# Kernel optimization log

Measured on AMD Instinct MI355X. Metric: run time of the kernel, lower is better.

Reference implementation:

```python
import jax, jax.numpy as jnp
import numpy as np
import math

B, H, M, L, D = 4, 8, 512, 2048, 64   # batch, heads, block len, span, head dim
RAMP = 64                              # adapt_span_len (soft-mask ramp size)


def setup_inputs() -> dict:
    key = jax.random.key(0)
    ks = jax.random.split(key, 5)
    BH = B * H
    KL = M + L
    return {
        "query": jax.random.normal(ks[0], (BH, M, D), jnp.float32),
        "key_": jax.random.normal(ks[1], (BH, KL, D), jnp.float32),
        "value": jax.random.normal(ks[2], (BH, KL, D), jnp.float32),
        "key_pe": jax.random.normal(ks[3], (1, D, L), jnp.float32) * 0.02,
        "current_val": jax.random.uniform(ks[4], (H, 1, 1), jnp.float32, minval=0.3, maxval=0.9),
    }


def reference(query, key_, value, key_pe, current_val):
    BH, Mq, Dh = query.shape
    KL = key_.shape[1]
    Lw = KL - Mq  # attention span
    nb = BH // current_val.shape[0]  # batch size (heads folded into leading dim)

    # full scores then unskew: band[b, i, j] = scores[b, i, i + j]
    scores = jnp.einsum('bmd,bnd->bmn', query, key_)              # (BH, M, M+L)
    rows = jnp.arange(Mq)[:, None]                                # (M, 1)
    band_idx = rows + jnp.arange(Lw)[None, :]                     # (M, L)
    attn = scores[:, rows, band_idx]                              # (BH, M, L)

    # relative position bias, scale, softmax
    attn = attn + jnp.einsum('bmd,dl->bml', query, key_pe[0])
    attn = attn / math.sqrt(Dh)
    attn = jax.nn.softmax(attn, axis=-1)

    # adaptive span soft mask (per head) + renormalization
    template = jnp.arange(1 - Lw, 1, dtype=attn.dtype)            # (L,) = linspace(1-L, 0, L)
    mask = jnp.clip((template + current_val * Lw) / RAMP + 1.0, 0.0, 1.0)  # (H, 1, L)
    attn4 = attn.reshape(nb, -1, Mq, Lw) * mask[None]             # (B, H, M, L)
    attn4 = attn4 / (attn4.sum(-1, keepdims=True) + 1e-8)
    attn = attn4.reshape(BH, Mq, Lw)

    # skew back to (BH, M, M+L) and contract with values
    skewed = jnp.zeros((BH, Mq, KL), attn.dtype).at[:, rows, band_idx].set(attn)
    out = jnp.einsum('bmn,bnd->bmd', skewed, value)               # (BH, M, D)
    return out
```

## Files before the change

### kernel.cpp

```cpp
#include <hip/hip_runtime.h>
#include <math.h>

typedef _Float16 half_t;
typedef _Float16 half8 __attribute__((ext_vector_type(8)));
typedef _Float16 half4 __attribute__((ext_vector_type(4)));
typedef _Float16 half2v __attribute__((ext_vector_type(2)));
typedef float f32x2 __attribute__((ext_vector_type(2)));
typedef float f32x4 __attribute__((ext_vector_type(4)));
typedef float f32x16 __attribute__((ext_vector_type(16)));
typedef unsigned int uint4v __attribute__((ext_vector_type(4)));

#define MFMA_S(a, b, c) __builtin_amdgcn_mfma_f32_32x32x16_f16((a), (b), (c), 0, 0, 0)

static constexpr int kM  = 512;
static constexpr int kD  = 64;
static constexpr int kKL = 2560;
static constexpr int kL  = 2048;
static constexpr int WS_VC  = 0;
static constexpr int WS_PET = WS_VC + 5242880;
static constexpr size_t WS_ZP_B = 10747904;
static constexpr size_t WS_PO_B = WS_ZP_B + 262144;

__global__ __launch_bounds__(256) void prep_tr(const float* __restrict__ v,
    const float* __restrict__ pe, half_t* __restrict__ ws) {
  __shared__ float ls[64 * 72];
  const int b = blockIdx.x, t = threadIdx.x;
  const bool isV = (b < 1280);
  int bh = 0, kt = 0, b3 = 0;
  const float* src; int sstride;
  if (isV) {
    bh = b / 40; kt = b % 40;
    src = v + (size_t)(bh * 2560 + kt * 64) * 64; sstride = 64;
  } else {
    b3 = b - 1280;
    src = pe + (size_t)b3 * 64; sstride = 2048;
  }
  const int rr = t >> 4, cq = (t & 15) * 4;
#pragma unroll
  for (int p = 0; p < 4; ++p) {
    const float4 x = *(const float4*)(src + (size_t)(p * 16 + rr) * sstride + cq);
    *(float4*)(ls + (p * 16 + rr) * 72 + cq) = x;
  }
  __syncthreads();
  const int oc = t >> 2, ch = t & 3;
  half_t tmp[16];
#pragma unroll
  for (int i2 = 0; i2 < 16; ++i2) tmp[i2] = (half_t)ls[(ch * 16 + i2) * 72 + oc];
  half_t* o;
  if (isV) {
    o = ws + WS_VC + (size_t)bh * 163840 + ((kt << 1) + (ch >> 1)) * 2048 + oc * 32 + ((ch & 1) << 4);
  } else {
    o = ws + WS_PET + ((size_t)b3 * 64 + oc) * 64 + ch * 16;
  }
  ((int4*)o)[0] = ((int4*)tmp)[0];
  ((int4*)o)[1] = ((int4*)tmp)[1];
}

__global__ __launch_bounds__(256, 2) void attn_kernel(
    const float* __restrict__ qg, const float* __restrict__ kg,
    const half_t* __restrict__ ws, const float* __restrict__ cvp,
    float* __restrict__ po, float* __restrict__ zp) {

  __shared__ __align__(16) char smem[43008];
  half_t* lsh = (half_t*)smem;

  const int tid  = threadIdx.x;
  const int lane = tid & 63;
  const int w    = tid >> 6;
  const int c32  = lane & 31;
  const int h    = lane >> 5;

  const int id = blockIdx.x;
  const int bh = ((id & 7) << 2) | (id >> 7);
  const int mid = (id >> 3) & 15;
  const int mb = mid & 3, sp = mid >> 2;
  const int m0 = mb << 7;
  const int g0 = sp * 17;

  const float cvl = cvp[bh & 7] * 2048.0f - 2047.0f;
  const float cvO = cvl * 0.015625f + 1.0f;

  const float*  kbF = kg + (size_t)bh * (kKL * kD);
  const half_t* vcb = ws + WS_VC + (size_t)bh * (kKL * kD);
  const half_t* pet = ws + WS_PET;

  const float QS = 0.125f * 1.4426950408889634f;
  const float* qrowF = qg + (size_t)(bh * kM + m0 + 32 * w + c32) * kD;
  half8 bq[4];
#pragma unroll
  for (int t = 0; t < 4; ++t) {
    const float4 qa = *(const float4*)(qrowF + t * 16 + h * 8);
    const float4 qb = *(const float4*)(qrowF + t * 16 + h * 8 + 4);
    bq[t] = half8{ (half_t)(qa.x * QS), (half_t)(qa.y * QS),
                   (half_t)(qa.z * QS), (half_t)(qa.w * QS),
                   (half_t)(qb.x * QS), (half_t)(qb.y * QS),
                   (half_t)(qb.z * QS), (half_t)(qb.w * QS) };
  }

  float* stfF = (float*)(smem + 9216) + w * 2112 + c32 * 66;

  float4 stgKa, stgKb;
  auto issueK = [&](int gg) {
    const int r = tid >> 3, seg = tid & 7;
    const int krow = m0 + (gg << 5) + r;
    const float* kp = kbF + (size_t)krow * kD + seg * 8;
    stgKa = *(const float4*)kp;
    stgKb = *(const float4*)(kp + 4);
  };
  auto commitK = [&](int gg) {
    const int sK = (gg & 1) * 2304;
    const int r = tid >> 3, seg = tid & 7;
    half_t tk[8];
    tk[0] = (half_t)stgKa.x; tk[1] = (half_t)stgKa.y;
    tk[2] = (half_t)stgKa.z; tk[3] = (half_t)stgKa.w;
    tk[4] = (half_t)stgKb.x; tk[5] = (half_t)stgKb.y;
    tk[6] = (half_t)stgKb.z; tk[7] = (half_t)stgKb.w;
    *(int4*)(lsh + sK + r * 72 + seg * 8) = *(int4*)tk;
  };

  auto loadV = [&](int gg, int4* vf) {
    const half_t* vp = vcb + (size_t)((m0 >> 5) + gg) * 2048;
#pragma unroll
    for (int dh = 0; dh < 2; ++dh)
#pragma unroll
      for (int kt = 0; kt < 2; ++kt)
        vf[dh * 2 + kt] = *(const int4*)(vp + (32 * dh + c32) * 32 + kt * 16 + h * 8);
  };

  auto petLoad = [&](int wb, half8* p) {
    int l = wb + c32; l = l < 0 ? 0 : (l > kL - 1 ? kL - 1 : l);
    const half_t* pp = pet + (size_t)l * kD;
#pragma unroll
    for (int t = 0; t < 4; ++t) p[t] = *(const half8*)(pp + t * 16 + h * 8);
  };
  auto peMFMA = [&](const half8* p) -> f32x16 {
    f32x16 a = {};
#pragma unroll
    for (int t = 0; t < 4; ++t) a = MFMA_S(p[t], bq[t], a);
    return a;
  };
  auto stripWrite = [&](int wb, const f32x16& a) {
    const int allone  = (wb >= 0) && (wb + 31 <= kL - 1) && (wb + cvl >= 0.0f);
    const int allzero = (wb > kL - 1) || (wb + 31 < 0) || ((float)(wb + 31) + cvl <= -64.0f);
#pragma unroll
    for (int reg = 0; reg < 16; ++reg) {
      const int lr = (reg & 3) + 8 * (reg >> 2) + 4 * h;
      const int l  = wb + lr;
      float bl;
      if (allzero) bl = -HUGE_VALF;
      else if (allone) bl = a[reg];
      else {
        const float mk = fminf(fmaxf((float)l * 0.015625f + cvO, 0.0f), 1.0f);
        const float lg = __builtin_amdgcn_logf(mk);
        bl = ((unsigned)l < (unsigned)kL) ? a[reg] + lg : -HUGE_VALF;
      }
      stfF[(l + c32) & 63] = bl;
    }
  };

  issueK(g0);
  const int B0 = (g0 << 5) - 32 * w;
  {
    half8 pq[4];
    petLoad(B0 - 32, pq); stripWrite(B0 - 32, peMFMA(pq));
    petLoad(B0,      pq); stripWrite(B0,      peMFMA(pq));
  }
  commitK(g0);
  __syncthreads();

  float zmc = 0.0f;
  f32x16 o0 = {}, o1 = {};

  half8 pp[4];
  int4 vf[4];
  for (int t = 0; t < 17; ++t) {
    const int g = g0 + t;
    const bool more = (t < 16);
    const int B = (g << 5) - 32 * w;
    if (more) {
      issueK(g + 1);
      petLoad(B + 32, pp);
    }
    loadV(g, vf);

    const int sK = (g & 1) * 2304;

    f32x16 s;
#pragma unroll
    for (int q = 0; q < 4; ++q) {
      const int base = (B + 8 * q + 4 * h) & 63;
      const f32x2 lo = *(const f32x2*)(stfF + base);
      const f32x2 hi = *(const f32x2*)(stfF + base + 2);
      s[4 * q + 0] = lo.x; s[4 * q + 1] = lo.y;
      s[4 * q + 2] = hi.x; s[4 * q + 3] = hi.y;
    }

    half8 ak[4];
#pragma unroll
    for (int kt = 0; kt < 4; ++kt)
      ak[kt] = *(const half8*)(lsh + sK + c32 * 72 + kt * 16 + h * 8);

#pragma unroll
    for (int kt = 0; kt < 4; ++kt) s = MFMA_S(ak[kt], bq[kt], s);

    float pm[16];
#pragma unroll
    for (int reg = 0; reg < 16; ++reg) pm[reg] = __builtin_amdgcn_exp2f(s[reg]);
    {
      const float t0 = (pm[0] + pm[1]) + (pm[2] + pm[3]);
      const float t1 = (pm[4] + pm[5]) + (pm[6] + pm[7]);
      const float t2 = (pm[8] + pm[9]) + (pm[10] + pm[11]);
      const float t3 = (pm[12] + pm[13]) + (pm[14] + pm[15]);
      zmc += (t0 + t1) + (t2 + t3);
    }
    unsigned Wp[8];
#pragma unroll
    for (int q = 0; q < 8; ++q)
      Wp[q] = __builtin_bit_cast(unsigned,
                __builtin_amdgcn_cvt_pkrtz(pm[2 * q], pm[2 * q + 1]));
    const auto r0 = __builtin_amdgcn_permlane32_swap(Wp[0], Wp[2], false, false);
    const auto r1 = __builtin_amdgcn_permlane32_swap(Wp[1], Wp[3], false, false);
    const auto r2 = __builtin_amdgcn_permlane32_swap(Wp[4], Wp[6], false, false);
    const auto r3 = __builtin_amdgcn_permlane32_swap(Wp[5], Wp[7], false, false);
    const uint4v u0 = { (unsigned)r0[0], (unsigned)r1[0], (unsigned)r0[1], (unsigned)r1[1] };
    const uint4v u1 = { (unsigned)r2[0], (unsigned)r3[0], (unsigned)r2[1], (unsigned)r3[1] };
    const half8 pb0 = __builtin_bit_cast(half8, u0);
    const half8 pb1 = __builtin_bit_cast(half8, u1);

    o0 = MFMA_S(__builtin_bit_cast(half8, vf[0]), pb0, o0);
    o0 = MFMA_S(__builtin_bit_cast(half8, vf[1]), pb1, o0);
    o1 = MFMA_S(__builtin_bit_cast(half8, vf[2]), pb0, o1);
    o1 = MFMA_S(__builtin_bit_cast(half8, vf[3]), pb1, o1);

    if (more) {
      stripWrite(B + 32, peMFMA(pp));
      commitK(g + 1);
    }
    __syncthreads();
  }

  float* Ow = (float*)smem + (size_t)w * 2176;
#pragma unroll
  for (int q = 0; q < 4; ++q) {
    *(f32x4*)(Ow + c32 * 68 + 0  + 8 * q + 4 * h) =
        f32x4{o0[q * 4], o0[q * 4 + 1], o0[q * 4 + 2], o0[q * 4 + 3]};
    *(f32x4*)(Ow + c32 * 68 + 32 + 8 * q + 4 * h) =
        f32x4{o1[q * 4], o1[q * 4 + 1], o1[q * 4 + 2], o1[q * 4 + 3]};
  }
  zmc += __shfl_xor(zmc, 32);
  const int rowbase = bh * kM + m0 + 32 * w;
  if (lane < 32) zp[(size_t)sp * 16384 + rowbase + c32] = zmc;
  __syncthreads();
  float* pob = po + ((size_t)sp * 16384 + rowbase) * 64;
#pragma unroll
  for (int u = 0; u < 8; ++u) {
    const int row = u * 4 + (lane >> 4);
    const int d4 = (lane & 15) << 2;
    *(f32x4*)(pob + (size_t)row * 64 + d4) = *(const f32x4*)(Ow + row * 68 + d4);
  }
}

__global__ __launch_bounds__(256) void norm_kernel(const float* __restrict__ zp,
    const float* __restrict__ po, float* __restrict__ out) {
  const int i = blockIdx.x * 256 + threadIdx.x;
  const int row = i >> 4, d4 = (i & 15) << 2;
  const float z = zp[row] + zp[16384 + row] + zp[32768 + row] + zp[49152 + row];
  const float inv = 1.0f / (z + 1e-20f);
  f32x4 a = *(const f32x4*)(po + (size_t)row * 64 + d4);
  const f32x4 b = *(const f32x4*)(po + 1048576u + (size_t)row * 64 + d4);
  const f32x4 c = *(const f32x4*)(po + 2097152u + (size_t)row * 64 + d4);
  const f32x4 d = *(const f32x4*)(po + 3145728u + (size_t)row * 64 + d4);
  a = a + b + c + d;
  *(f32x4*)(out + (size_t)row * 64 + d4) = a * inv;
}

extern "C" void kernel_launch(void* const* d_in, const int* in_sizes, int n_in,
                              void* d_out, int out_size, void* d_ws, size_t ws_size,
                              hipStream_t stream) {
  (void)in_sizes; (void)n_in; (void)out_size; (void)ws_size;
  const float* q  = (const float*)d_in[0];
  const float* k  = (const float*)d_in[1];
  const float* v  = (const float*)d_in[2];
  const float* pe = (const float*)d_in[3];
  const float* cv = (const float*)d_in[4];
  half_t* ws = (half_t*)d_ws;
  float* out = (float*)d_out;
  float* zp = (float*)((char*)d_ws + WS_ZP_B);
  float* po = (float*)((char*)d_ws + WS_PO_B);

  prep_tr<<<1312, 256, 0, stream>>>(v, pe, ws);
  attn_kernel<<<512, 256, 0, stream>>>(q, k, ws, cv, po, zp);
  norm_kernel<<<1024, 256, 0, stream>>>(zp, po, out);
}
```

Baseline: 133.6 us.

## Pre-convert K to fp16 and register-double-buffer K/V without per-step barriers

Adds a prep kernel that converts all of K to fp16 in the workspace. The attention kernel now loads K fragments straight from global into registers instead of staging them through shared memory. The main loop is unrolled by two with ping-pong register buffers for K, V and the position-embedding fragments, which removes the per-iteration __syncthreads. The cost is an extra kernel launch, a full extra read and write pass over K, and higher register pressure. K rows are also re-read from global/L2 by each wave instead of being shared through LDS.

```diff
diff --git a/kernel.cpp b/kernel.cpp
--- a/kernel.cpp
+++ b/kernel.cpp
@@ -16,10 +16,24 @@
 static constexpr int kD  = 64;
 static constexpr int kKL = 2560;
 static constexpr int kL  = 2048;
-static constexpr int WS_VC  = 0;
+static constexpr int WS_KH  = 0;
+static constexpr int WS_VC  = 5242880;
 static constexpr int WS_PET = WS_VC + 5242880;
-static constexpr size_t WS_ZP_B = 10747904;
+static constexpr size_t WS_ZP_B = 21233664;
 static constexpr size_t WS_PO_B = WS_ZP_B + 262144;
+
+__global__ __launch_bounds__(256) void prep_kc(const float* __restrict__ k,
+    half_t* __restrict__ ws) {
+  const int i = blockIdx.x * 256 + threadIdx.x;
+  const float* src = k + (size_t)i * 8;
+  half_t* dst = ws + WS_KH + (size_t)i * 8;
+  const float4 a = ((const float4*)src)[0];
+  const float4 b = ((const float4*)src)[1];
+  half_t tt[8];
+  tt[0] = (half_t)a.x; tt[1] = (half_t)a.y; tt[2] = (half_t)a.z; tt[3] = (half_t)a.w;
+  tt[4] = (half_t)b.x; tt[5] = (half_t)b.y; tt[6] = (half_t)b.z; tt[7] = (half_t)b.w;
+  *(int4*)dst = *(int4*)tt;
+}
 
 __global__ __launch_bounds__(256) void prep_tr(const float* __restrict__ v,
     const float* __restrict__ pe, half_t* __restrict__ ws) {
@@ -57,12 +71,11 @@
 }
 
 __global__ __launch_bounds__(256, 2) void attn_kernel(
-    const float* __restrict__ qg, const float* __restrict__ kg,
-    const half_t* __restrict__ ws, const float* __restrict__ cvp,
-    float* __restrict__ po, float* __restrict__ zp) {
-
-  __shared__ __align__(16) char smem[43008];
-  half_t* lsh = (half_t*)smem;
+    const float* __restrict__ qg, const half_t* __restrict__ ws,
+    const float* __restrict__ cvp, float* __restrict__ po,
+    float* __restrict__ zp) {
+
+  __shared__ __align__(16) char smem[34816];
 
   const int tid  = threadIdx.x;
   const int lane = tid & 63;
@@ -80,7 +93,7 @@
   const float cvl = cvp[bh & 7] * 2048.0f - 2047.0f;
   const float cvO = cvl * 0.015625f + 1.0f;
 
-  const float*  kbF = kg + (size_t)bh * (kKL * kD);
+  const half_t* khb = ws + WS_KH + (size_t)bh * (kKL * kD);
   const half_t* vcb = ws + WS_VC + (size_t)bh * (kKL * kD);
   const half_t* pet = ws + WS_PET;
 
@@ -97,37 +110,22 @@
                    (half_t)(qb.z * QS), (half_t)(qb.w * QS) };
   }
 
-  float* stfF = (float*)(smem + 9216) + w * 2112 + c32 * 66;
-
-  float4 stgKa, stgKb;
-  auto issueK = [&](int gg) {
-    const int r = tid >> 3, seg = tid & 7;
-    const int krow = m0 + (gg << 5) + r;
-    const float* kp = kbF + (size_t)krow * kD + seg * 8;
-    stgKa = *(const float4*)kp;
-    stgKb = *(const float4*)(kp + 4);
-  };
-  auto commitK = [&](int gg) {
-    const int sK = (gg & 1) * 2304;
-    const int r = tid >> 3, seg = tid & 7;
-    half_t tk[8];
-    tk[0] = (half_t)stgKa.x; tk[1] = (half_t)stgKa.y;
-    tk[2] = (half_t)stgKa.z; tk[3] = (half_t)stgKa.w;
-    tk[4] = (half_t)stgKb.x; tk[5] = (half_t)stgKb.y;
-    tk[6] = (half_t)stgKb.z; tk[7] = (half_t)stgKb.w;
-    *(int4*)(lsh + sK + r * 72 + seg * 8) = *(int4*)tk;
-  };
-
-  auto loadV = [&](int gg, int4* vf) {
-    const half_t* vp = vcb + (size_t)((m0 >> 5) + gg) * 2048;
+  float* stfF = (float*)smem + w * 2112 + c32 * 66;
+
+  auto loadK = [&](int gg, half8* ak) {
+    const half_t* kp = khb + (size_t)(m0 + (gg << 5) + c32) * kD + h * 8;
+#pragma unroll
+    for (int kt = 0; kt < 4; ++kt) ak[kt] = *(const half8*)(kp + kt * 16);
+  };
+  auto loadV = [&](int gg, half8* vf) {
+    const half_t* vp = vcb + (size_t)((m0 >> 5) + gg) * 2048 + h * 8;
 #pragma unroll
     for (int dh = 0; dh < 2; ++dh)
 #pragma unroll
       for (int kt = 0; kt < 2; ++kt)
-        vf[dh * 2 + kt] = *(const int4*)(vp + (32 * dh + c32) * 32 + kt * 16 + h * 8);
-  };
-
-  auto petLoad = [&](int wb, half8* p) {
+        vf[dh * 2 + kt] = *(const half8*)(vp + (32 * dh + c32) * 32 + kt * 16);
+  };
+  auto petL = [&](int wb, half8* p) {
     int l = wb + c32; l = l < 0 ? 0 : (l > kL - 1 ? kL - 1 : l);
     const half_t* pp = pet + (size_t)l * kD;
 #pragma unroll
@@ -158,33 +156,10 @@
     }
   };
 
-  issueK(g0);
-  const int B0 = (g0 << 5) - 32 * w;
-  {
-    half8 pq[4];
-    petLoad(B0 - 32, pq); stripWrite(B0 - 32, peMFMA(pq));
-    petLoad(B0,      pq); stripWrite(B0,      peMFMA(pq));
-  }
-  commitK(g0);
-  __syncthreads();
-
   float zmc = 0.0f;
   f32x16 o0 = {}, o1 = {};
 
-  half8 pp[4];
-  int4 vf[4];
-  for (int t = 0; t < 17; ++t) {
-    const int g = g0 + t;
-    const bool more = (t < 16);
-    const int B = (g << 5) - 32 * w;
-    if (more) {
-      issueK(g + 1);
-      petLoad(B + 32, pp);
-    }
-    loadV(g, vf);
-
-    const int sK = (g & 1) * 2304;
-
+  auto doStep = [&](int B, const half8* ak, const half8* vf) {
     f32x16 s;
 #pragma unroll
     for (int q = 0; q < 4; ++q) {
@@ -194,11 +169,6 @@
       s[4 * q + 0] = lo.x; s[4 * q + 1] = lo.y;
       s[4 * q + 2] = hi.x; s[4 * q + 3] = hi.y;
     }
-
-    half8 ak[4];
-#pragma unroll
-    for (int kt = 0; kt < 4; ++kt)
-      ak[kt] = *(const half8*)(lsh + sK + c32 * 72 + kt * 16 + h * 8);
 
 #pragma unroll
     for (int kt = 0; kt < 4; ++kt) s = MFMA_S(ak[kt], bq[kt], s);
@@ -227,18 +197,39 @@
     const half8 pb0 = __builtin_bit_cast(half8, u0);
     const half8 pb1 = __builtin_bit_cast(half8, u1);
 
-    o0 = MFMA_S(__builtin_bit_cast(half8, vf[0]), pb0, o0);
-    o0 = MFMA_S(__builtin_bit_cast(half8, vf[1]), pb1, o0);
-    o1 = MFMA_S(__builtin_bit_cast(half8, vf[2]), pb0, o1);
-    o1 = MFMA_S(__builtin_bit_cast(half8, vf[3]), pb1, o1);
-
-    if (more) {
-      stripWrite(B + 32, peMFMA(pp));
-      commitK(g + 1);
-    }
-    __syncthreads();
-  }
-
+    o0 = MFMA_S(vf[0], pb0, o0);
+    o0 = MFMA_S(vf[1], pb1, o0);
+    o1 = MFMA_S(vf[2], pb0, o1);
+    o1 = MFMA_S(vf[3], pb1, o1);
+  };
+
+  half8 akA[4], akB[4], vfA[4], vfB[4], ppA[4], ppB[4];
+  const int B0 = (g0 << 5) - 32 * w;
+  loadK(g0, akA); loadV(g0, vfA);
+  {
+    half8 pq[4];
+    petL(B0 - 32, pq); stripWrite(B0 - 32, peMFMA(pq));
+    petL(B0,      pq); stripWrite(B0,      peMFMA(pq));
+  }
+  petL(B0 + 32, ppA);
+
+  for (int p = 0; p < 8; ++p) {
+    const int g = g0 + 2 * p;
+    const int B = (g << 5) - 32 * w;
+
+    loadK(g + 1, akB); loadV(g + 1, vfB);
+    petL(B + 64, ppB);
+    doStep(B, akA, vfA);
+    stripWrite(B + 32, peMFMA(ppA));
+    const int B2 = B + 32;
+    loadK(g + 2, akA); loadV(g + 2, vfA);
+    if (p < 7) petL(B2 + 64, ppA);
+    doStep(B2, akB, vfB);
+    stripWrite(B2 + 32, peMFMA(ppB));
+  }
+  doStep(((g0 + 16) << 5) - 32 * w, akA, vfA);
+
+  __syncthreads();
   float* Ow = (float*)smem + (size_t)w * 2176;
 #pragma unroll
   for (int q = 0; q < 4; ++q) {
@@ -288,7 +279,8 @@
   float* zp = (float*)((char*)d_ws + WS_ZP_B);
   float* po = (float*)((char*)d_ws + WS_PO_B);
 
+  prep_kc<<<2560, 256, 0, stream>>>(k, ws);
   prep_tr<<<1312, 256, 0, stream>>>(v, pe, ws);
-  attn_kernel<<<512, 256, 0, stream>>>(q, k, ws, cv, po, zp);
+  attn_kernel<<<512, 256, 0, stream>>>(q, ws, cv, po, zp);
   norm_kernel<<<1024, 256, 0, stream>>>(zp, po, out);
 }
```

Result: slower. 142.3 us (+6.5%).
